# Optimization experiments

Measured on AMD Instinct MI355X. Metric: run time of the kernel, lower is better.

Reference implementation:

```python
import jax, jax.numpy as jnp
import numpy as np

NUM_HEADS = 16
HIDDEN = 1024
ATTN_DIM = 64            # per-head q/k dim
HEAD_OUT = 64            # per-head v dim
OUT_DIM = 1024
BATCH, SEQ = 2, 2048


def setup_inputs() -> dict:
    key = jax.random.key(0)
    ks = jax.random.split(key, 9)
    s_in = 1.0 / np.sqrt(HIDDEN)
    s_o = 1.0 / np.sqrt(NUM_HEADS * HEAD_OUT)
    return {
        "x": jax.random.normal(ks[0], (BATCH, SEQ, HIDDEN), dtype=jnp.float32),
        # Linear weights stored [in, out] so y = x @ W + b
        "Wq": jax.random.uniform(ks[1], (HIDDEN, NUM_HEADS * ATTN_DIM), jnp.float32, -s_in, s_in),
        "bq": jax.random.uniform(ks[2], (NUM_HEADS * ATTN_DIM,), jnp.float32, -s_in, s_in),
        "Wk": jax.random.uniform(ks[3], (HIDDEN, NUM_HEADS * ATTN_DIM), jnp.float32, -s_in, s_in),
        "bk": jax.random.uniform(ks[4], (NUM_HEADS * ATTN_DIM,), jnp.float32, -s_in, s_in),
        "Wv": jax.random.uniform(ks[5], (HIDDEN, NUM_HEADS * HEAD_OUT), jnp.float32, -s_in, s_in),
        "bv": jax.random.uniform(ks[6], (HIDDEN, NUM_HEADS * HEAD_OUT)[1:], jnp.float32, -s_in, s_in),
        "Wo": jax.random.uniform(ks[7], (NUM_HEADS * HEAD_OUT, OUT_DIM), jnp.float32, -s_o, s_o),
        "bo": jax.random.uniform(ks[8], (OUT_DIM,), jnp.float32, -s_o, s_o),
    }


def _split_heads(y, h):
    b, s, _ = y.shape
    return y.reshape(b, s, h, -1).transpose(0, 2, 1, 3)  # [b, h, s, d]


def reference(x, Wq, bq, Wk, bk, Wv, bv, Wo, bo):
    h = NUM_HEADS
    q = _split_heads(x @ Wq + bq, h)                    # [b,h,s,dq]
    k = _split_heads(x @ Wk + bk, h)                    # [b,h,s,dq]
    v = _split_heads(x @ Wv + bv, h)                    # [b,h,s,dv]
    scale = 1.0 / jnp.sqrt(jnp.float32(ATTN_DIM))
    # pattern[b,h,i,j] = key_i . query_j  (i=key index, j=query index)
    pattern = jnp.einsum('bhid,bhjd->bhij', k, q) * scale
    # softmax over key axis (dim=-2), matching t.softmax(..., dim=-2)
    prob = jax.nn.softmax(pattern, axis=-2)             # [b,h,key,query]
    # out[b,h,s,d] = sum_i prob[b,h,i,s] * v[b,h,i,d]
    out = jnp.einsum('bhis,bhid->bhsd', prob, v)        # [b,h,s,dv]
    b, _, s, dv = out.shape
    concat = out.transpose(0, 2, 1, 3).reshape(b, s, h * dv)
    return concat @ Wo + bo
```

## Files before the change

kernel.cpp:

```cpp
#include <hip/hip_runtime.h>
#include <cstdint>
#include <cstddef>

using f16   = _Float16;
using f16x4 = __attribute__((ext_vector_type(4))) _Float16;
using f16x8 = __attribute__((ext_vector_type(8))) _Float16;
using f32x4 = __attribute__((ext_vector_type(4))) float;

__device__ __forceinline__ f32x4 mfma16(f16x8 a, f16x8 b, f32x4 c) {
  return __builtin_amdgcn_mfma_f32_16x16x32_f16(a, b, c, 0, 0, 0);
}

__device__ __forceinline__ void gld16(const f16* g, f16* l) {
  __builtin_amdgcn_global_load_lds(
      (__attribute__((address_space(1))) void*)g,
      (__attribute__((address_space(3))) void*)l, 16, 0, 0);
}

constexpr int BATCH = 2, SEQL = 2048, HID = 1024, NH = 16, DH = 64;
constexpr int TOK = BATCH * SEQL;
constexpr int NQKV = 3 * HID;

__global__ __launch_bounds__(256) void k_convert_x(const float* __restrict__ x,
                                                   f16* __restrict__ xh) {
  int i = (blockIdx.x * 256 + threadIdx.x) * 4;
  float4 v = *(const float4*)(x + i);
  f16x4 o = { (f16)v.x, (f16)v.y, (f16)v.z, (f16)v.w };
  *(f16x4*)(xh + i) = o;
}

__global__ __launch_bounds__(256) void k_transpose(const float* __restrict__ Wq,
                                                   const float* __restrict__ Wk,
                                                   const float* __restrict__ Wv,
                                                   const float* __restrict__ Wo,
                                                   f16* __restrict__ WT,
                                                   f16* __restrict__ WoT) {
  __shared__ float tile[32][33];
  int mat = blockIdx.z;
  const float* W = (mat == 0) ? Wq : (mat == 1) ? Wk : (mat == 2) ? Wv : Wo;
  int in0 = blockIdx.x * 32, out0 = blockIdx.y * 32;
  int c = threadIdx.x & 31, r8 = threadIdx.x >> 5;
#pragma unroll
  for (int i = 0; i < 4; i++) {
    int r = r8 + i * 8;
    tile[r][c] = W[(size_t)(in0 + r) * HID + out0 + c];
  }
  __syncthreads();
#pragma unroll
  for (int i = 0; i < 4; i++) {
    int r = r8 + i * 8;
    f16 v = (f16)tile[c][r];
    if (mat == 3) WoT[(size_t)(out0 + r) * HID + in0 + c] = v;
    else          WT[(size_t)(mat * HID + out0 + r) * HID + in0 + c] = v;
  }
}

__global__ __launch_bounds__(256, 2) void k_gemm_qkv(
    const f16* __restrict__ xh, const f16* __restrict__ WT,
    const float* __restrict__ bq, const float* __restrict__ bk,
    const float* __restrict__ bv,
    f16* __restrict__ Qh, f16* __restrict__ Kh, f16* __restrict__ Vp) {
  constexpr int K = HID;
  int m0 = blockIdx.x * 128, n0 = blockIdx.y * 128;
  int tid = threadIdx.x;
  int w = tid >> 6, lane = tid & 63, lr = lane & 15, lq = lane >> 4;
  int wm = w >> 1, wn = w & 1;
  __shared__ f16 Ash[128 * 32];
  __shared__ f16 Bsh[128 * 32];
  f32x4 acc[4][4];
#pragma unroll
  for (int i = 0; i < 4; i++)
#pragma unroll
    for (int j = 0; j < 4; j++) acc[i][j] = (f32x4){0.f, 0.f, 0.f, 0.f};

  int row0 = tid >> 2, seg0 = tid & 3;
  int row1 = (256 + tid) >> 2;
  const f16* Ag0 = xh + (size_t)(m0 + row0) * K + seg0 * 8;
  const f16* Ag1 = xh + (size_t)(m0 + row1) * K + seg0 * 8;
  const f16* Bg0 = WT + (size_t)(n0 + row0) * K + seg0 * 8;
  const f16* Bg1 = WT + (size_t)(n0 + row1) * K + seg0 * 8;

  for (int k0 = 0; k0 < K; k0 += 32) {
    __syncthreads();
    gld16(Ag0 + k0, Ash + tid * 8);
    gld16(Ag1 + k0, Ash + (256 + tid) * 8);
    gld16(Bg0 + k0, Bsh + tid * 8);
    gld16(Bg1 + k0, Bsh + (256 + tid) * 8);
    __syncthreads();
    f16x8 af[4], bfr[4];
#pragma unroll
    for (int mt = 0; mt < 4; mt++)
      af[mt] = *(const f16x8*)(Ash + (wm * 64 + mt * 16 + lr) * 32 + lq * 8);
#pragma unroll
    for (int nt = 0; nt < 4; nt++)
      bfr[nt] = *(const f16x8*)(Bsh + (wn * 64 + nt * 16 + lr) * 32 + lq * 8);
#pragma unroll
    for (int mt = 0; mt < 4; mt++)
#pragma unroll
      for (int nt = 0; nt < 4; nt++)
        acc[mt][nt] = mfma16(af[mt], bfr[nt], acc[mt][nt]);
  }

#pragma unroll
  for (int nt = 0; nt < 4; nt++) {
    int o = n0 + wn * 64 + nt * 16 + lr;
    int sec = o >> 10, o1 = o & 1023, hh = o1 >> 6, dd = o1 & 63;
    float bias = (sec == 0) ? bq[o1] : (sec == 1) ? bk[o1] : bv[o1];
#pragma unroll
    for (int mt = 0; mt < 4; mt++) {
      int t0 = m0 + wm * 64 + mt * 16 + lq * 4;
      int b = t0 >> 11, s0 = t0 & (SEQL - 1);
      size_t bh = (size_t)(b * NH + hh);
      if (sec == 2) {
        f16x4 pv = { (f16)(acc[mt][nt][0] + bias), (f16)(acc[mt][nt][1] + bias),
                     (f16)(acc[mt][nt][2] + bias), (f16)(acc[mt][nt][3] + bias) };
        int pb = (s0 & ~31) | ((s0 & 12) << 1) | ((s0 >> 2) & 4);
        *(f16x4*)(Vp + (bh * DH + dd) * SEQL + pb) = pv;
      } else {
        f16* dst = (sec == 0) ? Qh : Kh;
#pragma unroll
        for (int r = 0; r < 4; r++)
          dst[(bh * SEQL + s0 + r) * DH + dd] = (f16)(acc[mt][nt][r] + bias);
      }
    }
  }
}

__global__ __launch_bounds__(512, 2) void k_attn(const f16* __restrict__ Qh,
                                                 const f16* __restrict__ Kh,
                                                 const f16* __restrict__ Vp,
                                                 f16* __restrict__ Ao) {
  int bh = blockIdx.x;
  int qblk = blockIdx.y;
  int b = bh >> 4, h = bh & 15;
  int tid = threadIdx.x;
  int w = tid >> 6;
  int g = w >> 2;
  int wq = w & 3;
  int lane = tid & 63, lr = lane & 15, lq = lane >> 4;

  __shared__ f16 sh[8 * 64 * 72];

  f16x8 qf[4][2];
#pragma unroll
  for (int qt = 0; qt < 4; qt++) {
    const f16* Qbase =
        Qh + ((size_t)bh * SEQL + qblk * 256 + wq * 64 + qt * 16 + lr) * DH;
#pragma unroll
    for (int ks = 0; ks < 2; ks++) {
      qf[qt][ks] = *(const f16x8*)(Qbase + ks * 32 + lq * 8);
      qf[qt][ks] = qf[qt][ks] * (f16)0.18033688f;
    }
  }

  f32x4 O[4][4];
#pragma unroll
  for (int qt = 0; qt < 4; qt++)
#pragma unroll
    for (int dt = 0; dt < 4; dt++) O[qt][dt] = (f32x4){0.f, 0.f, 0.f, 0.f};
  float lsum[4] = {0.f, 0.f, 0.f, 0.f};

  int gtid = tid & 255;
  int srow = gtid >> 3, sseg = gtid & 7, srow1 = srow + 32;
  int kbase = g * 1024;
  const f16* Kg0 = Kh + ((size_t)bh * SEQL + kbase + srow) * DH + sseg * 8;
  const f16* Kg1 = Kh + ((size_t)bh * SEQL + kbase + srow1) * DH + sseg * 8;
  const f16* Vg0 = Vp + ((size_t)bh * DH + srow) * SEQL + kbase + sseg * 8;
  const f16* Vg1 = Vp + ((size_t)bh * DH + srow1) * SEQL + kbase + sseg * 8;

  uint4 kr0 = *(const uint4*)(Kg0), kr1 = *(const uint4*)(Kg1);
  uint4 vr0 = *(const uint4*)(Vg0), vr1 = *(const uint4*)(Vg1);

  for (int kb = 0; kb < 16; kb++) {
    f16* Kp = sh + ((g * 2 + (kb & 1)) * 2 + 0) * 4608;
    f16* Vq = Kp + 4608;
    *(uint4*)(Kp + srow * 72 + sseg * 8) = kr0;
    *(uint4*)(Kp + srow1 * 72 + sseg * 8) = kr1;
    *(uint4*)(Vq + srow * 72 + sseg * 8) = vr0;
    *(uint4*)(Vq + srow1 * 72 + sseg * 8) = vr1;
    if (kb < 15) {
      size_t ko = (size_t)(kb + 1) * 64 * DH;
      int vo = (kb + 1) * 64;
      kr0 = *(const uint4*)(Kg0 + ko);
      kr1 = *(const uint4*)(Kg1 + ko);
      vr0 = *(const uint4*)(Vg0 + vo);
      vr1 = *(const uint4*)(Vg1 + vo);
    }
    __syncthreads();

    f32x4 sacc[4][4];
#pragma unroll
    for (int qt = 0; qt < 4; qt++)
#pragma unroll
      for (int kt = 0; kt < 4; kt++) sacc[qt][kt] = (f32x4){0.f, 0.f, 0.f, 0.f};
#pragma unroll
    for (int ks = 0; ks < 2; ks++) {
#pragma unroll
      for (int kt = 0; kt < 4; kt++) {
        f16x8 kf = *(const f16x8*)(Kp + (kt * 16 + lr) * 72 + ks * 32 + lq * 8);
        sacc[0][kt] = mfma16(kf, qf[0][ks], sacc[0][kt]);
        sacc[1][kt] = mfma16(kf, qf[1][ks], sacc[1][kt]);
        sacc[2][kt] = mfma16(kf, qf[2][ks], sacc[2][kt]);
        sacc[3][kt] = mfma16(kf, qf[3][ks], sacc[3][kt]);
      }
    }

    f16x8 pf[4][2];
#pragma unroll
    for (int qt = 0; qt < 4; qt++) {
      float part = 0.f;
#pragma unroll
      for (int kt = 0; kt < 4; kt++) {
        float p0 = __builtin_amdgcn_exp2f(sacc[qt][kt][0]);
        float p1 = __builtin_amdgcn_exp2f(sacc[qt][kt][1]);
        float p2 = __builtin_amdgcn_exp2f(sacc[qt][kt][2]);
        float p3 = __builtin_amdgcn_exp2f(sacc[qt][kt][3]);
        part += (p0 + p1) + (p2 + p3);
        int s = kt >> 1, off = (kt & 1) * 4;
        pf[qt][s][off + 0] = (f16)p0; pf[qt][s][off + 1] = (f16)p1;
        pf[qt][s][off + 2] = (f16)p2; pf[qt][s][off + 3] = (f16)p3;
      }
      lsum[qt] += part;
    }

#pragma unroll
    for (int s = 0; s < 2; s++) {
#pragma unroll
      for (int dt = 0; dt < 4; dt++) {
        f16x8 vf = *(const f16x8*)(Vq + (dt * 16 + lr) * 72 + s * 32 + lq * 8);
        O[0][dt] = mfma16(vf, pf[0][s], O[0][dt]);
        O[1][dt] = mfma16(vf, pf[1][s], O[1][dt]);
        O[2][dt] = mfma16(vf, pf[2][s], O[2][dt]);
        O[3][dt] = mfma16(vf, pf[3][s], O[3][dt]);
      }
    }
  }

  __syncthreads();
  float* part = (float*)sh;
  float* plsum = part + 16384;
  if (g == 1) {
#pragma unroll
    for (int qt = 0; qt < 4; qt++) {
      int ql = wq * 64 + qt * 16 + lr;
#pragma unroll
      for (int dt = 0; dt < 4; dt++) {
        int slot = (dt * 4 + lq) ^ lr;
        *(f32x4*)(part + ql * 64 + slot * 4) = O[qt][dt];
      }
      plsum[ql * 4 + lq] = lsum[qt];
    }
  }
  __syncthreads();
  if (g == 0) {
#pragma unroll
    for (int qt = 0; qt < 4; qt++) {
      int ql = wq * 64 + qt * 16 + lr;
      float ls = lsum[qt] + plsum[ql * 4 + lq];
      float l1 = ls + __shfl_xor(ls, 16);
      float ltot = l1 + __shfl_xor(l1, 32);
      float inv = 1.0f / ltot;
      int q = qblk * 256 + ql;
      f16* dst = Ao + ((size_t)b * SEQL + q) * HID + h * DH;
#pragma unroll
      for (int dt = 0; dt < 4; dt++) {
        int slot = (dt * 4 + lq) ^ lr;
        f32x4 po = *(const f32x4*)(part + ql * 64 + slot * 4);
        f16x4 o = { (f16)((O[qt][dt][0] + po[0]) * inv),
                    (f16)((O[qt][dt][1] + po[1]) * inv),
                    (f16)((O[qt][dt][2] + po[2]) * inv),
                    (f16)((O[qt][dt][3] + po[3]) * inv) };
        *(f16x4*)(dst + dt * 16 + lq * 4) = o;
      }
    }
  }
}

__global__ __launch_bounds__(256, 2) void k_gemm_out(const f16* __restrict__ Ah,
                                                     const f16* __restrict__ WoT,
                                                     const float* __restrict__ bo,
                                                     float* __restrict__ out) {
  constexpr int K = HID;
  int m0 = blockIdx.x * 128, n0 = blockIdx.y * 64;
  int tid = threadIdx.x;
  int w = tid >> 6, lane = tid & 63, lr = lane & 15, lq = lane >> 4;
  int wm = w >> 1, wn = w & 1;
  __shared__ f16 Ash[128 * 32];
  __shared__ f16 Bsh[64 * 32];
  f32x4 acc[4][2];
#pragma unroll
  for (int i = 0; i < 4; i++)
#pragma unroll
    for (int j = 0; j < 2; j++) acc[i][j] = (f32x4){0.f, 0.f, 0.f, 0.f};

  int row0 = tid >> 2, seg0 = tid & 3;
  int row1 = (256 + tid) >> 2;
  const f16* Ag0 = Ah + (size_t)(m0 + row0) * K + seg0 * 8;
  const f16* Ag1 = Ah + (size_t)(m0 + row1) * K + seg0 * 8;
  const f16* Bg0 = WoT + (size_t)(n0 + row0) * K + seg0 * 8;

  for (int k0 = 0; k0 < K; k0 += 32) {
    __syncthreads();
    gld16(Ag0 + k0, Ash + tid * 8);
    gld16(Ag1 + k0, Ash + (256 + tid) * 8);
    gld16(Bg0 + k0, Bsh + tid * 8);
    __syncthreads();
    f16x8 af[4], bfr[2];
#pragma unroll
    for (int mt = 0; mt < 4; mt++)
      af[mt] = *(const f16x8*)(Ash + (wm * 64 + mt * 16 + lr) * 32 + lq * 8);
#pragma unroll
    for (int nt = 0; nt < 2; nt++)
      bfr[nt] = *(const f16x8*)(Bsh + (wn * 32 + nt * 16 + lr) * 32 + lq * 8);
#pragma unroll
    for (int mt = 0; mt < 4; mt++)
#pragma unroll
      for (int nt = 0; nt < 2; nt++)
        acc[mt][nt] = mfma16(af[mt], bfr[nt], acc[mt][nt]);
  }

#pragma unroll
  for (int nt = 0; nt < 2; nt++) {
    int o = n0 + wn * 32 + nt * 16 + lr;
    float bias = bo[o];
#pragma unroll
    for (int mt = 0; mt < 4; mt++) {
      int t0 = m0 + wm * 64 + mt * 16 + lq * 4;
#pragma unroll
      for (int r = 0; r < 4; r++)
        out[(size_t)(t0 + r) * HID + o] = acc[mt][nt][r] + bias;
    }
  }
}

extern "C" void kernel_launch(void* const* d_in, const int* in_sizes, int n_in,
                              void* d_out, int out_size, void* d_ws, size_t ws_size,
                              hipStream_t stream) {
  const float* x  = (const float*)d_in[0];
  const float* Wq = (const float*)d_in[1];
  const float* bq = (const float*)d_in[2];
  const float* Wk = (const float*)d_in[3];
  const float* bk = (const float*)d_in[4];
  const float* Wv = (const float*)d_in[5];
  const float* bv = (const float*)d_in[6];
  const float* Wo = (const float*)d_in[7];
  const float* bo = (const float*)d_in[8];

  char* ws = (char*)d_ws;
  f16* xh  = (f16*)(ws + 0);
  f16* WT  = (f16*)(ws + 8388608);
  f16* WoT = (f16*)(ws + 14680064);
  f16* Qh  = (f16*)(ws + 16777216);
  f16* Kh  = (f16*)(ws + 25165824);
  f16* Vp  = (f16*)(ws + 33554432);
  f16* Ao  = (f16*)(ws + 41943040);

  k_convert_x<<<TOK * HID / 1024, 256, 0, stream>>>(x, xh);
  k_transpose<<<dim3(32, 32, 4), 256, 0, stream>>>(Wq, Wk, Wv, Wo, WT, WoT);
  k_gemm_qkv<<<dim3(TOK / 128, NQKV / 128), 256, 0, stream>>>(xh, WT, bq, bk, bv,
                                                              Qh, Kh, Vp);
  k_attn<<<dim3(BATCH * NH, SEQL / 256), 512, 0, stream>>>(Qh, Kh, Vp, Ao);
  k_gemm_out<<<dim3(TOK / 128, HID / 64), 256, 0, stream>>>(Ao, WoT, bo,
                                                            (float*)d_out);
}
```

Measured before the change: 179.8 us.

## Halve attention block to 128 queries and prioritize MFMA sections with setprio

The attention kernel now runs 256 threads per block covering 128 queries instead of 256, doubling the grid to 512 blocks. Each thread loads four K/V rows per tile instead of two. s_setprio raises wave priority around the QK and PV MFMA loops. The smaller blocks are meant to improve occupancy and load balance, at the cost of loading each K/V tile twice as often per query.

Result: slower. 230.9 us (+28.4%).

```diff
diff --git a/kernel.cpp b/kernel.cpp
--- a/kernel.cpp
+++ b/kernel.cpp
@@ -126,7 +126,7 @@
   }
 }
 
-__global__ __launch_bounds__(512, 2) void k_attn(const f16* __restrict__ Qh,
+__global__ __launch_bounds__(256, 2) void k_attn(const f16* __restrict__ Qh,
                                                  const f16* __restrict__ Kh,
                                                  const f16* __restrict__ Vp,
                                                  f16* __restrict__ Ao) {
@@ -135,8 +135,8 @@
   int b = bh >> 4, h = bh & 15;
   int tid = threadIdx.x;
   int w = tid >> 6;
-  int g = w >> 2;
-  int wq = w & 3;
+  int g = w >> 1;
+  int wq = w & 1;
   int lane = tid & 63, lr = lane & 15, lq = lane >> 4;
 
   __shared__ f16 sh[8 * 64 * 72];
@@ -145,7 +145,7 @@
 #pragma unroll
   for (int qt = 0; qt < 4; qt++) {
     const f16* Qbase =
-        Qh + ((size_t)bh * SEQL + qblk * 256 + wq * 64 + qt * 16 + lr) * DH;
+        Qh + ((size_t)bh * SEQL + qblk * 128 + wq * 64 + qt * 16 + lr) * DH;
 #pragma unroll
     for (int ks = 0; ks < 2; ks++) {
       qf[qt][ks] = *(const f16x8*)(Qbase + ks * 32 + lq * 8);
@@ -160,31 +160,35 @@
     for (int dt = 0; dt < 4; dt++) O[qt][dt] = (f32x4){0.f, 0.f, 0.f, 0.f};
   float lsum[4] = {0.f, 0.f, 0.f, 0.f};
 
-  int gtid = tid & 255;
-  int srow = gtid >> 3, sseg = gtid & 7, srow1 = srow + 32;
+  int gtid = tid & 127;
+  int srow = gtid >> 3, sseg = gtid & 7;
   int kbase = g * 1024;
-  const f16* Kg0 = Kh + ((size_t)bh * SEQL + kbase + srow) * DH + sseg * 8;
-  const f16* Kg1 = Kh + ((size_t)bh * SEQL + kbase + srow1) * DH + sseg * 8;
-  const f16* Vg0 = Vp + ((size_t)bh * DH + srow) * SEQL + kbase + sseg * 8;
-  const f16* Vg1 = Vp + ((size_t)bh * DH + srow1) * SEQL + kbase + sseg * 8;
-
-  uint4 kr0 = *(const uint4*)(Kg0), kr1 = *(const uint4*)(Kg1);
-  uint4 vr0 = *(const uint4*)(Vg0), vr1 = *(const uint4*)(Vg1);
+  const f16* Kg = Kh + ((size_t)bh * SEQL + kbase + srow) * DH + sseg * 8;
+  const f16* Vg = Vp + ((size_t)bh * DH + srow) * SEQL + kbase + sseg * 8;
+
+  uint4 kr[4], vr[4];
+#pragma unroll
+  for (int r = 0; r < 4; r++) {
+    kr[r] = *(const uint4*)(Kg + (size_t)(16 * r) * DH);
+    vr[r] = *(const uint4*)(Vg + (size_t)(16 * r) * SEQL);
+  }
 
   for (int kb = 0; kb < 16; kb++) {
-    f16* Kp = sh + ((g * 2 + (kb & 1)) * 2 + 0) * 4608;
+    f16* Kp = sh + ((g * 2 + (kb & 1)) * 2) * 4608;
     f16* Vq = Kp + 4608;
-    *(uint4*)(Kp + srow * 72 + sseg * 8) = kr0;
-    *(uint4*)(Kp + srow1 * 72 + sseg * 8) = kr1;
-    *(uint4*)(Vq + srow * 72 + sseg * 8) = vr0;
-    *(uint4*)(Vq + srow1 * 72 + sseg * 8) = vr1;
+#pragma unroll
+    for (int r = 0; r < 4; r++) {
+      *(uint4*)(Kp + (srow + 16 * r) * 72 + sseg * 8) = kr[r];
+      *(uint4*)(Vq + (srow + 16 * r) * 72 + sseg * 8) = vr[r];
+    }
     if (kb < 15) {
       size_t ko = (size_t)(kb + 1) * 64 * DH;
       int vo = (kb + 1) * 64;
-      kr0 = *(const uint4*)(Kg0 + ko);
-      kr1 = *(const uint4*)(Kg1 + ko);
-      vr0 = *(const uint4*)(Vg0 + vo);
-      vr1 = *(const uint4*)(Vg1 + vo);
+#pragma unroll
+      for (int r = 0; r < 4; r++) {
+        kr[r] = *(const uint4*)(Kg + ko + (size_t)(16 * r) * DH);
+        vr[r] = *(const uint4*)(Vg + vo + (size_t)(16 * r) * SEQL);
+      }
     }
     __syncthreads();
 
@@ -193,6 +197,7 @@
     for (int qt = 0; qt < 4; qt++)
 #pragma unroll
       for (int kt = 0; kt < 4; kt++) sacc[qt][kt] = (f32x4){0.f, 0.f, 0.f, 0.f};
+    __builtin_amdgcn_s_setprio(1);
 #pragma unroll
     for (int ks = 0; ks < 2; ks++) {
 #pragma unroll
@@ -204,6 +209,7 @@
         sacc[3][kt] = mfma16(kf, qf[3][ks], sacc[3][kt]);
       }
     }
+    __builtin_amdgcn_s_setprio(0);
 
     f16x8 pf[4][2];
 #pragma unroll
@@ -223,6 +229,7 @@
       lsum[qt] += part;
     }
 
+    __builtin_amdgcn_s_setprio(1);
 #pragma unroll
     for (int s = 0; s < 2; s++) {
 #pragma unroll
@@ -234,11 +241,12 @@
         O[3][dt] = mfma16(vf, pf[3][s], O[3][dt]);
       }
     }
+    __builtin_amdgcn_s_setprio(0);
   }
 
   __syncthreads();
   float* part = (float*)sh;
-  float* plsum = part + 16384;
+  float* plsum = part + 128 * 64;
   if (g == 1) {
 #pragma unroll
     for (int qt = 0; qt < 4; qt++) {
@@ -260,7 +268,7 @@
       float l1 = ls + __shfl_xor(ls, 16);
       float ltot = l1 + __shfl_xor(l1, 32);
       float inv = 1.0f / ltot;
-      int q = qblk * 256 + ql;
+      int q = qblk * 128 + ql;
       f16* dst = Ao + ((size_t)b * SEQL + q) * HID + h * DH;
 #pragma unroll
       for (int dt = 0; dt < 4; dt++) {
@@ -359,7 +367,7 @@
   k_transpose<<<dim3(32, 32, 4), 256, 0, stream>>>(Wq, Wk, Wv, Wo, WT, WoT);
   k_gemm_qkv<<<dim3(TOK / 128, NQKV / 128), 256, 0, stream>>>(xh, WT, bq, bk, bv,
                                                               Qh, Kh, Vp);
-  k_attn<<<dim3(BATCH * NH, SEQL / 256), 512, 0, stream>>>(Qh, Kh, Vp, Ao);
+  k_attn<<<dim3(BATCH * NH, SEQL / 128), 256, 0, stream>>>(Qh, Kh, Vp, Ao);
   k_gemm_out<<<dim3(TOK / 128, HID / 64), 256, 0, stream>>>(Ao, WoT, bo,
                                                             (float*)d_out);
 }
```
